# Kernel optimization log

Hardware: AMD Instinct MI355X
Metric: run time of the kernel (lower is better)

The kernel has to match this reference:

```python
import jax, jax.numpy as jnp
import numpy as np

B, S, F, OWN, H, E = 16384, 37, 17, 9, 256, 128
NOUT = 7 + 16


def setup_inputs() -> dict:
    key = jax.random.key(0)
    ks = jax.random.split(key, 22)
    obs = jax.random.normal(ks[0], (B, S + 1, F), dtype=jnp.float32)
    pad = jax.random.bernoulli(ks[1], 0.3, (B, S))
    obs = obs.at[:, 1:, :].multiply(jnp.where(pad, 0.0, 1.0)[:, :, None])

    def init(k, shape):
        return jax.random.normal(k, shape, dtype=jnp.float32) * 0.05

    params = dict(
        sW1=init(ks[2], (F, H)), sb1=jnp.zeros((H,), jnp.float32),
        sW2=init(ks[3], (H, H)), sb2=jnp.zeros((H,), jnp.float32),
        sW3=init(ks[4], (H, E)), sb3=jnp.zeros((E,), jnp.float32),
        aW1=init(ks[5], (E + OWN, H)), ab1=jnp.zeros((H,), jnp.float32),
        aW2=init(ks[6], (H, H)), ab2=jnp.zeros((H,), jnp.float32),
        aW3=init(ks[7], (H, NOUT)), ab3=jnp.zeros((NOUT,), jnp.float32),
        vW1=init(ks[8], (E + OWN, H)), vb1=jnp.zeros((H,), jnp.float32),
        vW2=init(ks[9], (H, H)), vb2=jnp.zeros((H,), jnp.float32),
        vW3=init(ks[10], (H, 1)), vb3=jnp.zeros((1,), jnp.float32),
    )
    return {"obs": obs, **params}


def reference(obs, sW1, sb1, sW2, sb2, sW3, sb3,
              aW1, ab1, aW2, ab2, aW3, ab3,
              vW1, vb1, vW2, vb2, vW3, vb3):
    s_own = obs[:, 0, :OWN]                      # [B, 9]
    seqs = obs[:, 1:, :]                         # [B, 37, 17]
    # non-padded mask: rows whose abs-sum is nonzero
    mask = (jnp.sum(jnp.abs(seqs), axis=-1) != 0).astype(obs.dtype)  # [B, 37]

    # shared MLP applied to every row; masked positions zeroed before the
    # pooling sum (equivalent to gather->MLP->scatter into zeros->sum)
    h = jax.nn.relu(seqs @ sW1 + sb1)
    h = jax.nn.relu(h @ sW2 + sb2)
    h = jax.nn.relu(h @ sW3 + sb3)               # [B, 37, E]
    h = h * mask[..., None]
    summed = jnp.sum(h, axis=1)                  # [B, E]

    cat = jnp.concatenate([summed, s_own], axis=1)  # [B, E+9]

    a = jax.nn.relu(cat @ aW1 + ab1)
    a = jax.nn.relu(a @ aW2 + ab2)
    action_logits = a @ aW3 + ab3                # [B, 23]

    v = jax.nn.relu(cat @ vW1 + vb1)
    v = jax.nn.relu(v @ vW2 + vb2)
    value = (v @ vW3 + vb3).reshape(-1)          # [B]

    return action_logits, value
```

## Files before the change

kernel.cpp:

```cpp
#include <hip/hip_runtime.h>
#include <hip/hip_bf16.h>

#define B_    16384
#define S_    37
#define F_    17
#define OWN_  9
#define NOUT_ 23
#define OBS_ROW 646

typedef __bf16 bf16x8 __attribute__((ext_vector_type(8)));
typedef float  f32x4  __attribute__((ext_vector_type(4)));

#define MFMA(a,b,c) __builtin_amdgcn_mfma_f32_16x16x32_bf16(a, b, c, 0, 0, 0)

#define W1F_OFF   0
#define W2F_OFF   8192
#define W3F_OFF   73728
#define AW1F_OFF  106496
#define AW2F_OFF  147456
#define AW3F_OFF  212992
#define VW1F_OFF  221184
#define VW2F_OFF  262144
#define VW3F_OFF  327680
#define PREP_TOTAL 331776

__global__ void prep_kernel(const float* __restrict__ sW1, const float* __restrict__ sW2,
                            const float* __restrict__ sW3, const float* __restrict__ aW1,
                            const float* __restrict__ aW2, const float* __restrict__ aW3,
                            const float* __restrict__ vW1, const float* __restrict__ vW2,
                            const float* __restrict__ vW3, __bf16* __restrict__ ws)
{
    int j = blockIdx.x * 256 + threadIdx.x;
    const float* src; __bf16* dst; int Np, Ks, Ns;
    if (j < 8192)                  { dst = ws + W1F_OFF;  src = sW1; Np = 256; Ks = 17;  Ns = 256; }
    else if ((j -= 8192)  < 65536) { dst = ws + W2F_OFF;  src = sW2; Np = 256; Ks = 256; Ns = 256; }
    else if ((j -= 65536) < 32768) { dst = ws + W3F_OFF;  src = sW3; Np = 128; Ks = 256; Ns = 128; }
    else if ((j -= 32768) < 40960) { dst = ws + AW1F_OFF; src = aW1; Np = 256; Ks = 137; Ns = 256; }
    else if ((j -= 40960) < 65536) { dst = ws + AW2F_OFF; src = aW2; Np = 256; Ks = 256; Ns = 256; }
    else if ((j -= 65536) < 8192)  { dst = ws + AW3F_OFF; src = aW3; Np = 32;  Ks = 256; Ns = 23;  }
    else if ((j -= 8192)  < 40960) { dst = ws + VW1F_OFF; src = vW1; Np = 256; Ks = 137; Ns = 256; }
    else if ((j -= 40960) < 65536) { dst = ws + VW2F_OFF; src = vW2; Np = 256; Ks = 256; Ns = 256; }
    else { j -= 65536;               dst = ws + VW3F_OFF; src = vW3; Np = 16;  Ks = 256; Ns = 1;   }
    const int c = j / (Np * 8), rem = j - c * Np * 8, n = rem >> 3, e = rem & 7, k = c * 8 + e;
    const float v = (k < Ks && n < Ns) ? src[k * Ns + n] : 0.f;
    dst[j] = (__bf16)v;
}

__global__ __launch_bounds__(512, 2) void fused_kernel(
    const float* __restrict__ obs,
    const float* __restrict__ sb1, const float* __restrict__ sb2, const float* __restrict__ sb3,
    const float* __restrict__ ab1, const float* __restrict__ ab2, const float* __restrict__ ab3,
    const float* __restrict__ vb1, const float* __restrict__ vb2, const float* __restrict__ vb3,
    const __bf16* __restrict__ ws, float* __restrict__ out)
{
    __shared__ __align__(16) char pool[74240];
    __bf16* act1 = (__bf16*)pool;
    __bf16* act2 = (__bf16*)(pool + 32768);
    __bf16* xs0  = (__bf16*)(pool + 65536);
    __bf16* xs1  = (__bf16*)(pool + 69632);
    float*  sm0  = (float*)(pool + 73728);
    float*  sm1  = (float*)(pool + 73984);
    __bf16* catf = (__bf16*)(pool + 65536);

    const __bf16* W1f  = ws + W1F_OFF;
    const __bf16* W2f  = ws + W2F_OFF;
    const __bf16* W3f  = ws + W3F_OFF;
    const __bf16* AW1f = ws + AW1F_OFF;
    const __bf16* AW2f = ws + AW2F_OFF;
    const __bf16* AW3f = ws + AW3F_OFF;
    const __bf16* VW1f = ws + VW1F_OFF;
    const __bf16* VW2f = ws + VW2F_OFF;
    const __bf16* VW3f = ws + VW3F_OFF;

    const int tid  = threadIdx.x;
    const int wave = tid >> 6;
    const int lane = tid & 63;
    const int q    = lane >> 4;
    const int l16  = lane & 15;
    const int b0   = blockIdx.x * 16;
    const f32x4 z4 = {0.f, 0.f, 0.f, 0.f};

    for (int i = tid; i < 4096; i += 512) xs0[i] = (__bf16)0.f;

    bf16x8 w1f[2], w2f[8][2], w3f[8];
    float b1v[2], b2v[2];
    #pragma unroll
    for (int nt = 0; nt < 2; ++nt) {
        const int n = wave * 32 + nt * 16 + l16;
        w1f[nt] = *(const bf16x8*)(W1f + ((size_t)q * 256 + n) * 8);
        b1v[nt] = sb1[n];
        b2v[nt] = sb2[n];
        #pragma unroll
        for (int k = 0; k < 8; ++k)
            w2f[k][nt] = *(const bf16x8*)(W2f + ((size_t)(k * 4 + q) * 256 + n) * 8);
    }
    #pragma unroll
    for (int k = 0; k < 8; ++k)
        w3f[k] = *(const bf16x8*)(W3f + ((size_t)(k * 4 + q) * 128 + wave * 16 + l16) * 8);
    const float b3v = sb3[wave * 16 + l16];

    __syncthreads();

    if (wave == 7) {
        const float* p = obs + (size_t)(b0 + (lane & 15)) * OBS_ROW + ((lane >> 4) + 1) * F_;
        float sm = 0.f;
        #pragma unroll
        for (int c = 0; c < F_; ++c) {
            const float v = p[c];
            sm += fabsf(v);
            xs0[((c >> 3) * 64 + lane) * 8 + (c & 7)] = (__bf16)v;
        }
        sm0[lane] = sm;
    }

    f32x4 vsum = z4;

    for (int it = 0; it < 10; ++it) {
        __bf16* xc  = (it & 1) ? xs1 : xs0;
        __bf16* xn  = (it & 1) ? xs0 : xs1;
        float*  smc = (it & 1) ? sm1 : sm0;
        float*  smn = (it & 1) ? sm0 : sm1;

        __syncthreads();

        if (it < 9 && wave == 7) {
            const int s = 4 * (it + 1) + (lane >> 4);
            if (s < S_) {
                const float* p = obs + (size_t)(b0 + (lane & 15)) * OBS_ROW + (s + 1) * F_;
                float sm = 0.f;
                #pragma unroll
                for (int c = 0; c < F_; ++c) {
                    const float v = p[c];
                    sm += fabsf(v);
                    xn[((c >> 3) * 64 + lane) * 8 + (c & 7)] = (__bf16)v;
                }
                smn[lane] = sm;
            } else {
                smn[lane] = 0.f;
            }
        }

        {
            #pragma unroll
            for (int m = 0; m < 4; ++m) {
                const bf16x8 af = *(const bf16x8*)(xc + (q * 64 + m * 16 + l16) * 8);
                #pragma unroll
                for (int nt = 0; nt < 2; ++nt) {
                    const f32x4 h = MFMA(af, w1f[nt], z4);
                    const int n = wave * 32 + nt * 16 + l16, c = n >> 3, e = n & 7;
                    #pragma unroll
                    for (int r = 0; r < 4; ++r) {
                        float v = h[r] + b1v[nt]; v = v > 0.f ? v : 0.f;
                        act1[(c * 64 + m * 16 + q * 4 + r) * 8 + e] = (__bf16)v;
                    }
                }
            }
        }
        __syncthreads();

        {
            f32x4 h2[2][4];
            #pragma unroll
            for (int nt = 0; nt < 2; ++nt)
                #pragma unroll
                for (int m = 0; m < 4; ++m) h2[nt][m] = z4;
            #pragma unroll
            for (int k = 0; k < 8; ++k) {
                const int k8 = k * 4 + q;
                #pragma unroll
                for (int m = 0; m < 4; ++m) {
                    const bf16x8 a = *(const bf16x8*)(act1 + (k8 * 64 + m * 16 + l16) * 8);
                    h2[0][m] = MFMA(a, w2f[k][0], h2[0][m]);
                    h2[1][m] = MFMA(a, w2f[k][1], h2[1][m]);
                }
            }
            #pragma unroll
            for (int nt = 0; nt < 2; ++nt) {
                const int n = wave * 32 + nt * 16 + l16, c = n >> 3, e = n & 7;
                #pragma unroll
                for (int m = 0; m < 4; ++m)
                    #pragma unroll
                    for (int r = 0; r < 4; ++r) {
                        float v = h2[nt][m][r] + b2v[nt]; v = v > 0.f ? v : 0.f;
                        act2[(c * 64 + m * 16 + q * 4 + r) * 8 + e] = (__bf16)v;
                    }
            }
        }
        __syncthreads();

        {
            f32x4 h3[4];
            #pragma unroll
            for (int m = 0; m < 4; ++m) h3[m] = z4;
            #pragma unroll
            for (int k = 0; k < 8; ++k) {
                const int k8 = k * 4 + q;
                #pragma unroll
                for (int m = 0; m < 4; ++m) {
                    const bf16x8 a = *(const bf16x8*)(act2 + (k8 * 64 + m * 16 + l16) * 8);
                    h3[m] = MFMA(a, w3f[k], h3[m]);
                }
            }
            #pragma unroll
            for (int m = 0; m < 4; ++m)
                #pragma unroll
                for (int r = 0; r < 4; ++r) {
                    const float mv = smc[m * 16 + q * 4 + r];
                    float v = h3[m][r] + b3v;
                    v = v > 0.f ? v : 0.f;
                    vsum[r] += (mv != 0.f) ? v : 0.f;
                }
    }
    }

    __syncthreads();

    if (tid < 16) {
        const float* p = obs + (size_t)(b0 + tid) * OBS_ROW;
        #pragma unroll
        for (int c = 0; c < 8; ++c) catf[(16 * 16 + tid) * 8 + c] = (__bf16)p[c];
        catf[(17 * 16 + tid) * 8 + 0] = (__bf16)p[8];
        #pragma unroll
        for (int c = 1; c < 8; ++c) catf[(17 * 16 + tid) * 8 + c] = (__bf16)0.f;
    } else if (tid < 32) {
        const int rr = tid - 16;
        #pragma unroll
        for (int c = 0; c < 8; ++c) {
            catf[(18 * 16 + rr) * 8 + c] = (__bf16)0.f;
            catf[(19 * 16 + rr) * 8 + c] = (__bf16)0.f;
        }
    }
    {
        const int col = wave * 16 + l16, c = col >> 3, e = col & 7;
        #pragma unroll
        for (int r = 0; r < 4; ++r)
            catf[(c * 16 + q * 4 + r) * 8 + e] = (__bf16)vsum[r];
    }
    __syncthreads();

    {
        f32x4 ha[2], hv[2];
        #pragma unroll
        for (int nt = 0; nt < 2; ++nt) { ha[nt] = z4; hv[nt] = z4; }
        #pragma unroll
        for (int k = 0; k < 5; ++k) {
            const int k8 = k * 4 + q;
            const bf16x8 ca = *(const bf16x8*)(catf + (k8 * 16 + l16) * 8);
            #pragma unroll
            for (int nt = 0; nt < 2; ++nt) {
                const int n = wave * 32 + nt * 16 + l16;
                const bf16x8 ba = *(const bf16x8*)(AW1f + ((size_t)k8 * 256 + n) * 8);
                const bf16x8 bv = *(const bf16x8*)(VW1f + ((size_t)k8 * 256 + n) * 8);
                ha[nt] = MFMA(ca, ba, ha[nt]);
                hv[nt] = MFMA(ca, bv, hv[nt]);
            }
        }
        #pragma unroll
        for (int nt = 0; nt < 2; ++nt) {
            const int n = wave * 32 + nt * 16 + l16, c = n >> 3, e = n & 7;
            const float ba_ = ab1[n], bv_ = vb1[n];
            #pragma unroll
            for (int r = 0; r < 4; ++r) {
                float va = ha[nt][r] + ba_; va = va > 0.f ? va : 0.f;
                float vv = hv[nt][r] + bv_; vv = vv > 0.f ? vv : 0.f;
                act1[(c * 64 + q * 4 + r) * 8 + e]      = (__bf16)va;
                act1[(c * 64 + 16 + q * 4 + r) * 8 + e] = (__bf16)vv;
            }
        }
    }
    __syncthreads();

    {
        f32x4 ha[2], hv[2];
        #pragma unroll
        for (int nt = 0; nt < 2; ++nt) { ha[nt] = z4; hv[nt] = z4; }
        #pragma unroll
        for (int k = 0; k < 8; ++k) {
            const int k8 = k * 4 + q;
            const bf16x8 a0 = *(const bf16x8*)(act1 + (k8 * 64 + l16) * 8);
            const bf16x8 a1 = *(const bf16x8*)(act1 + (k8 * 64 + 16 + l16) * 8);
            #pragma unroll
            for (int nt = 0; nt < 2; ++nt) {
                const int n = wave * 32 + nt * 16 + l16;
                const bf16x8 ba = *(const bf16x8*)(AW2f + ((size_t)k8 * 256 + n) * 8);
                const bf16x8 bv = *(const bf16x8*)(VW2f + ((size_t)k8 * 256 + n) * 8);
                ha[nt] = MFMA(a0, ba, ha[nt]);
                hv[nt] = MFMA(a1, bv, hv[nt]);
            }
        }
        #pragma unroll
        for (int nt = 0; nt < 2; ++nt) {
            const int n = wave * 32 + nt * 16 + l16, c = n >> 3, e = n & 7;
            const float ba_ = ab2[n], bv_ = vb2[n];
            #pragma unroll
            for (int r = 0; r < 4; ++r) {
                float va = ha[nt][r] + ba_; va = va > 0.f ? va : 0.f;
                float vv = hv[nt][r] + bv_; vv = vv > 0.f ? vv : 0.f;
                act2[(c * 64 + q * 4 + r) * 8 + e]      = (__bf16)va;
                act2[(c * 64 + 16 + q * 4 + r) * 8 + e] = (__bf16)vv;
            }
        }
    }
    __syncthreads();

    if (wave < 2) {
        f32x4 acc = z4;
        #pragma unroll
        for (int k = 0; k < 8; ++k) {
            const int k8 = k * 4 + q;
            const bf16x8 a0 = *(const bf16x8*)(act2 + (k8 * 64 + l16) * 8);
            const bf16x8 bf = *(const bf16x8*)(AW3f + ((size_t)k8 * 32 + wave * 16 + l16) * 8);
            acc = MFMA(a0, bf, acc);
        }
        const int col = wave * 16 + l16;
        if (col < NOUT_) {
            const float bb = ab3[col];
            #pragma unroll
            for (int r = 0; r < 4; ++r)
                out[(size_t)(b0 + q * 4 + r) * NOUT_ + col] = acc[r] + bb;
        }
    } else if (wave == 2) {
        f32x4 acc = z4;
        #pragma unroll
        for (int k = 0; k < 8; ++k) {
            const int k8 = k * 4 + q;
            const bf16x8 a1 = *(const bf16x8*)(act2 + (k8 * 64 + 16 + l16) * 8);
            const bf16x8 bf = *(const bf16x8*)(VW3f + ((size_t)k8 * 16 + l16) * 8);
            acc = MFMA(a1, bf, acc);
        }
        if (l16 == 0) {
            const float bb = vb3[0];
            #pragma unroll
            for (int r = 0; r < 4; ++r)
                out[(size_t)B_ * NOUT_ + b0 + q * 4 + r] = acc[r] + bb;
        }
    }
}

extern "C" void kernel_launch(void* const* d_in, const int* in_sizes, int n_in,
                              void* d_out, int out_size, void* d_ws, size_t ws_size,
                              hipStream_t stream)
{
    const float* obs = (const float*)d_in[0];
    const float* sW1 = (const float*)d_in[1];
    const float* sb1 = (const float*)d_in[2];
    const float* sW2 = (const float*)d_in[3];
    const float* sb2 = (const float*)d_in[4];
    const float* sW3 = (const float*)d_in[5];
    const float* sb3 = (const float*)d_in[6];
    const float* aW1 = (const float*)d_in[7];
    const float* ab1 = (const float*)d_in[8];
    const float* aW2 = (const float*)d_in[9];
    const float* ab2 = (const float*)d_in[10];
    const float* aW3 = (const float*)d_in[11];
    const float* ab3 = (const float*)d_in[12];
    const float* vW1 = (const float*)d_in[13];
    const float* vb1 = (const float*)d_in[14];
    const float* vW2 = (const float*)d_in[15];
    const float* vb2 = (const float*)d_in[16];
    const float* vW3 = (const float*)d_in[17];
    const float* vb3 = (const float*)d_in[18];

    __bf16* ws = (__bf16*)d_ws;
    float* out = (float*)d_out;

    hipLaunchKernelGGL(prep_kernel, dim3(PREP_TOTAL / 256), dim3(256), 0, stream,
                       sW1, sW2, sW3, aW1, aW2, aW3, vW1, vW2, vW3, ws);
    hipLaunchKernelGGL(fused_kernel, dim3(B_ / 16), dim3(512), 0, stream,
                       obs, sb1, sb2, sb3, ab1, ab2, ab3, vb1, vb2, vb3,
                       (const __bf16*)ws, out);
}
```

Baseline: 281.9 us.

## Switch MFMA operand order to row-major padded LDS layout and regroup wave tiling

Changes the shared-memory activation layout from chunked k8-major to row-major with padded row strides, so the bank-conflict pattern changes. MFMA operands are swapped so each lane writes four contiguous bf16 outputs as one vector store. The tiling is regrouped so each wave covers 64 output columns and 32 rows rather than 32 columns and 64 rows. Biases are staged in shared memory, and the actor and value heads are split across the two wave halves. The aim is cheaper LDS stores and fewer bank conflicts, at the cost of roughly twice the register-resident weight fragments per wave, which may hurt occupancy.

```diff
diff --git a/kernel.cpp b/kernel.cpp
--- a/kernel.cpp
+++ b/kernel.cpp
@@ -9,6 +9,7 @@
 #define OBS_ROW 646
 
 typedef __bf16 bf16x8 __attribute__((ext_vector_type(8)));
+typedef __bf16 bf16x4 __attribute__((ext_vector_type(4)));
 typedef float  f32x4  __attribute__((ext_vector_type(4)));
 
 #define MFMA(a,b,c) __builtin_amdgcn_mfma_f32_16x16x32_bf16(a, b, c, 0, 0, 0)
@@ -23,6 +24,10 @@
 #define VW2F_OFF  262144
 #define VW3F_OFF  327680
 #define PREP_TOTAL 331776
+
+#define RS_ACT 264
+#define RS_XS  40
+#define RS_CAT 168
 
 __global__ void prep_kernel(const float* __restrict__ sW1, const float* __restrict__ sW2,
                             const float* __restrict__ sW3, const float* __restrict__ aW1,
@@ -53,43 +58,37 @@
     const float* __restrict__ vb1, const float* __restrict__ vb2, const float* __restrict__ vb3,
     const __bf16* __restrict__ ws, float* __restrict__ out)
 {
-    __shared__ __align__(16) char pool[74240];
-    __bf16* act1 = (__bf16*)pool;
-    __bf16* act2 = (__bf16*)(pool + 32768);
-    __bf16* xs0  = (__bf16*)(pool + 65536);
-    __bf16* xs1  = (__bf16*)(pool + 69632);
-    float*  sm0  = (float*)(pool + 73728);
-    float*  sm1  = (float*)(pool + 73984);
-    __bf16* catf = (__bf16*)(pool + 65536);
+    __shared__ __align__(16) __bf16 act1[64 * RS_ACT];
+    __shared__ __align__(16) __bf16 act2[64 * RS_ACT];
+    __shared__ __align__(16) __bf16 xs[2][64 * RS_XS];
+    __shared__ float sm[2][64];
+    __shared__ __align__(16) float sbias[640];
+    __shared__ __align__(16) __bf16 catf[16 * RS_CAT];
 
     const __bf16* W1f  = ws + W1F_OFF;
     const __bf16* W2f  = ws + W2F_OFF;
     const __bf16* W3f  = ws + W3F_OFF;
-    const __bf16* AW1f = ws + AW1F_OFF;
-    const __bf16* AW2f = ws + AW2F_OFF;
-    const __bf16* AW3f = ws + AW3F_OFF;
-    const __bf16* VW1f = ws + VW1F_OFF;
-    const __bf16* VW2f = ws + VW2F_OFF;
-    const __bf16* VW3f = ws + VW3F_OFF;
 
     const int tid  = threadIdx.x;
     const int wave = tid >> 6;
     const int lane = tid & 63;
     const int q    = lane >> 4;
     const int l16  = lane & 15;
+    const int wg   = wave & 3;
+    const int th   = wave >> 2;
+    const int tb   = th * 32;
     const int b0   = blockIdx.x * 16;
     const f32x4 z4 = {0.f, 0.f, 0.f, 0.f};
 
-    for (int i = tid; i < 4096; i += 512) xs0[i] = (__bf16)0.f;
-
-    bf16x8 w1f[2], w2f[8][2], w3f[8];
-    float b1v[2], b2v[2];
+    for (int i = tid; i < 640; i += 512)
+        sbias[i] = (i < 256) ? sb1[i] : (i < 512 ? sb2[i - 256] : sb3[i - 512]);
+    for (int i = tid; i < 2 * 64 * RS_XS; i += 512) xs[0][i] = (__bf16)0.f;
+
+    bf16x8 w1f[4], w2f[8][4], w3f[8];
     #pragma unroll
-    for (int nt = 0; nt < 2; ++nt) {
-        const int n = wave * 32 + nt * 16 + l16;
+    for (int nt = 0; nt < 4; ++nt) {
+        const int n = wg * 64 + nt * 16 + l16;
         w1f[nt] = *(const bf16x8*)(W1f + ((size_t)q * 256 + n) * 8);
-        b1v[nt] = sb1[n];
-        b2v[nt] = sb2[n];
         #pragma unroll
         for (int k = 0; k < 8; ++k)
             w2f[k][nt] = *(const bf16x8*)(W2f + ((size_t)(k * 4 + q) * 256 + n) * 8);
@@ -97,93 +96,99 @@
     #pragma unroll
     for (int k = 0; k < 8; ++k)
         w3f[k] = *(const bf16x8*)(W3f + ((size_t)(k * 4 + q) * 128 + wave * 16 + l16) * 8);
-    const float b3v = sb3[wave * 16 + l16];
 
     __syncthreads();
 
     if (wave == 7) {
         const float* p = obs + (size_t)(b0 + (lane & 15)) * OBS_ROW + ((lane >> 4) + 1) * F_;
-        float sm = 0.f;
+        float smv = 0.f;
         #pragma unroll
         for (int c = 0; c < F_; ++c) {
             const float v = p[c];
-            sm += fabsf(v);
-            xs0[((c >> 3) * 64 + lane) * 8 + (c & 7)] = (__bf16)v;
-        }
-        sm0[lane] = sm;
-    }
+            smv += fabsf(v);
+            xs[0][lane * RS_XS + c] = (__bf16)v;
+        }
+        sm[0][lane] = smv;
+    }
+    __syncthreads();
 
     f32x4 vsum = z4;
 
     for (int it = 0; it < 10; ++it) {
-        __bf16* xc  = (it & 1) ? xs1 : xs0;
-        __bf16* xn  = (it & 1) ? xs0 : xs1;
-        float*  smc = (it & 1) ? sm1 : sm0;
-        float*  smn = (it & 1) ? sm0 : sm1;
-
-        __syncthreads();
+        const __bf16* xc = xs[it & 1];
+        __bf16*       xn = xs[1 - (it & 1)];
+        const float* smc = sm[it & 1];
+        float*       smn = sm[1 - (it & 1)];
 
         if (it < 9 && wave == 7) {
             const int s = 4 * (it + 1) + (lane >> 4);
             if (s < S_) {
                 const float* p = obs + (size_t)(b0 + (lane & 15)) * OBS_ROW + (s + 1) * F_;
-                float sm = 0.f;
+                float smv = 0.f;
                 #pragma unroll
                 for (int c = 0; c < F_; ++c) {
                     const float v = p[c];
-                    sm += fabsf(v);
-                    xn[((c >> 3) * 64 + lane) * 8 + (c & 7)] = (__bf16)v;
-                }
-                smn[lane] = sm;
+                    smv += fabsf(v);
+                    xn[lane * RS_XS + c] = (__bf16)v;
+                }
+                smn[lane] = smv;
             } else {
                 smn[lane] = 0.f;
             }
         }
 
         {
-            #pragma unroll
-            for (int m = 0; m < 4; ++m) {
-                const bf16x8 af = *(const bf16x8*)(xc + (q * 64 + m * 16 + l16) * 8);
-                #pragma unroll
-                for (int nt = 0; nt < 2; ++nt) {
-                    const f32x4 h = MFMA(af, w1f[nt], z4);
-                    const int n = wave * 32 + nt * 16 + l16, c = n >> 3, e = n & 7;
+            bf16x8 xa[2];
+            #pragma unroll
+            for (int tt = 0; tt < 2; ++tt)
+                xa[tt] = *(const bf16x8*)(xc + (tb + tt * 16 + l16) * RS_XS + q * 8);
+            #pragma unroll
+            for (int nt = 0; nt < 4; ++nt) {
+                const int n0 = wg * 64 + nt * 16 + q * 4;
+                const f32x4 bb = *(const f32x4*)(sbias + n0);
+                #pragma unroll
+                for (int tt = 0; tt < 2; ++tt) {
+                    const f32x4 h = MFMA(w1f[nt], xa[tt], z4);
+                    bf16x4 o;
                     #pragma unroll
                     for (int r = 0; r < 4; ++r) {
-                        float v = h[r] + b1v[nt]; v = v > 0.f ? v : 0.f;
-                        act1[(c * 64 + m * 16 + q * 4 + r) * 8 + e] = (__bf16)v;
+                        float v = h[r] + bb[r];
+                        o[r] = (__bf16)(v > 0.f ? v : 0.f);
                     }
+                    *(bf16x4*)(act1 + (tb + tt * 16 + l16) * RS_ACT + n0) = o;
                 }
             }
         }
         __syncthreads();
 
         {
-            f32x4 h2[2][4];
-            #pragma unroll
-            for (int nt = 0; nt < 2; ++nt)
-                #pragma unroll
-                for (int m = 0; m < 4; ++m) h2[nt][m] = z4;
+            f32x4 acc[4][2];
+            #pragma unroll
+            for (int nt = 0; nt < 4; ++nt) { acc[nt][0] = z4; acc[nt][1] = z4; }
             #pragma unroll
             for (int k = 0; k < 8; ++k) {
-                const int k8 = k * 4 + q;
-                #pragma unroll
-                for (int m = 0; m < 4; ++m) {
-                    const bf16x8 a = *(const bf16x8*)(act1 + (k8 * 64 + m * 16 + l16) * 8);
-                    h2[0][m] = MFMA(a, w2f[k][0], h2[0][m]);
-                    h2[1][m] = MFMA(a, w2f[k][1], h2[1][m]);
-                }
-            }
-            #pragma unroll
-            for (int nt = 0; nt < 2; ++nt) {
-                const int n = wave * 32 + nt * 16 + l16, c = n >> 3, e = n & 7;
-                #pragma unroll
-                for (int m = 0; m < 4; ++m)
+                const bf16x8 a0 = *(const bf16x8*)(act1 + (tb + l16) * RS_ACT + k * 32 + q * 8);
+                const bf16x8 a1 = *(const bf16x8*)(act1 + (tb + 16 + l16) * RS_ACT + k * 32 + q * 8);
+                #pragma unroll
+                for (int nt = 0; nt < 4; ++nt) {
+                    acc[nt][0] = MFMA(w2f[k][nt], a0, acc[nt][0]);
+                    acc[nt][1] = MFMA(w2f[k][nt], a1, acc[nt][1]);
+                }
+            }
+            #pragma unroll
+            for (int nt = 0; nt < 4; ++nt) {
+                const int n0 = wg * 64 + nt * 16 + q * 4;
+                const f32x4 bb = *(const f32x4*)(sbias + 256 + n0);
+                #pragma unroll
+                for (int tt = 0; tt < 2; ++tt) {
+                    bf16x4 o;
                     #pragma unroll
                     for (int r = 0; r < 4; ++r) {
-                        float v = h2[nt][m][r] + b2v[nt]; v = v > 0.f ? v : 0.f;
-                        act2[(c * 64 + m * 16 + q * 4 + r) * 8 + e] = (__bf16)v;
+                        float v = acc[nt][tt][r] + bb[r];
+                        o[r] = (__bf16)(v > 0.f ? v : 0.f);
                     }
+                    *(bf16x4*)(act2 + (tb + tt * 16 + l16) * RS_ACT + n0) = o;
+                }
             }
         }
         __syncthreads();
@@ -194,111 +199,100 @@
             for (int m = 0; m < 4; ++m) h3[m] = z4;
             #pragma unroll
             for (int k = 0; k < 8; ++k) {
-                const int k8 = k * 4 + q;
                 #pragma unroll
                 for (int m = 0; m < 4; ++m) {
-                    const bf16x8 a = *(const bf16x8*)(act2 + (k8 * 64 + m * 16 + l16) * 8);
-                    h3[m] = MFMA(a, w3f[k], h3[m]);
-                }
-            }
-            #pragma unroll
-            for (int m = 0; m < 4; ++m)
+                    const bf16x8 a = *(const bf16x8*)(act2 + (m * 16 + l16) * RS_ACT + k * 32 + q * 8);
+                    h3[m] = MFMA(w3f[k], a, h3[m]);
+                }
+            }
+            const f32x4 bb = *(const f32x4*)(sbias + 512 + wave * 16 + q * 4);
+            #pragma unroll
+            for (int m = 0; m < 4; ++m) {
+                const float mv = smc[m * 16 + l16];
                 #pragma unroll
                 for (int r = 0; r < 4; ++r) {
-                    const float mv = smc[m * 16 + q * 4 + r];
-                    float v = h3[m][r] + b3v;
+                    float v = h3[m][r] + bb[r];
                     v = v > 0.f ? v : 0.f;
                     vsum[r] += (mv != 0.f) ? v : 0.f;
                 }
-    }
-    }
-
-    __syncthreads();
-
+            }
+        }
+    }
+
+    {
+        bf16x4 o;
+        #pragma unroll
+        for (int r = 0; r < 4; ++r) o[r] = (__bf16)vsum[r];
+        *(bf16x4*)(catf + l16 * RS_CAT + wave * 16 + q * 4) = o;
+    }
     if (tid < 16) {
         const float* p = obs + (size_t)(b0 + tid) * OBS_ROW;
         #pragma unroll
-        for (int c = 0; c < 8; ++c) catf[(16 * 16 + tid) * 8 + c] = (__bf16)p[c];
-        catf[(17 * 16 + tid) * 8 + 0] = (__bf16)p[8];
-        #pragma unroll
-        for (int c = 1; c < 8; ++c) catf[(17 * 16 + tid) * 8 + c] = (__bf16)0.f;
-    } else if (tid < 32) {
-        const int rr = tid - 16;
-        #pragma unroll
-        for (int c = 0; c < 8; ++c) {
-            catf[(18 * 16 + rr) * 8 + c] = (__bf16)0.f;
-            catf[(19 * 16 + rr) * 8 + c] = (__bf16)0.f;
-        }
-    }
+        for (int j = 0; j < OWN_; ++j) catf[tid * RS_CAT + 128 + j] = (__bf16)p[j];
+        #pragma unroll
+        for (int j = OWN_; j < 32; ++j) catf[tid * RS_CAT + 128 + j] = (__bf16)0.f;
+    }
+    __syncthreads();
+
+    const bool  actor = (wave < 4);
+    const int   drow  = actor ? l16 : (16 + l16);
+    const __bf16* HW1 = ws + (actor ? AW1F_OFF : VW1F_OFF);
+    const __bf16* HW2 = ws + (actor ? AW2F_OFF : VW2F_OFF);
+    const float* hb1  = actor ? ab1 : vb1;
+    const float* hb2  = actor ? ab2 : vb2;
+
     {
-        const int col = wave * 16 + l16, c = col >> 3, e = col & 7;
-        #pragma unroll
-        for (int r = 0; r < 4; ++r)
-            catf[(c * 16 + q * 4 + r) * 8 + e] = (__bf16)vsum[r];
+        f32x4 acc[4];
+        #pragma unroll
+        for (int nt = 0; nt < 4; ++nt) acc[nt] = z4;
+        #pragma unroll
+        for (int k = 0; k < 5; ++k) {
+            const bf16x8 ca = *(const bf16x8*)(catf + l16 * RS_CAT + k * 32 + q * 8);
+            #pragma unroll
+            for (int nt = 0; nt < 4; ++nt) {
+                const bf16x8 wf = *(const bf16x8*)(HW1 + ((size_t)(k * 4 + q) * 256 + wg * 64 + nt * 16 + l16) * 8);
+                acc[nt] = MFMA(wf, ca, acc[nt]);
+            }
+        }
+        #pragma unroll
+        for (int nt = 0; nt < 4; ++nt) {
+            const int n0 = wg * 64 + nt * 16 + q * 4;
+            const f32x4 bb = *(const f32x4*)(hb1 + n0);
+            bf16x4 o;
+            #pragma unroll
+            for (int r = 0; r < 4; ++r) {
+                float v = acc[nt][r] + bb[r];
+                o[r] = (__bf16)(v > 0.f ? v : 0.f);
+            }
+            *(bf16x4*)(act1 + drow * RS_ACT + n0) = o;
+        }
     }
     __syncthreads();
 
     {
-        f32x4 ha[2], hv[2];
-        #pragma unroll
-        for (int nt = 0; nt < 2; ++nt) { ha[nt] = z4; hv[nt] = z4; }
-        #pragma unroll
-        for (int k = 0; k < 5; ++k) {
-            const int k8 = k * 4 + q;
-            const bf16x8 ca = *(const bf16x8*)(catf + (k8 * 16 + l16) * 8);
-            #pragma unroll
-            for (int nt = 0; nt < 2; ++nt) {
-                const int n = wave * 32 + nt * 16 + l16;
-                const bf16x8 ba = *(const bf16x8*)(AW1f + ((size_t)k8 * 256 + n) * 8);
-                const bf16x8 bv = *(const bf16x8*)(VW1f + ((size_t)k8 * 256 + n) * 8);
-                ha[nt] = MFMA(ca, ba, ha[nt]);
-                hv[nt] = MFMA(ca, bv, hv[nt]);
-            }
-        }
-        #pragma unroll
-        for (int nt = 0; nt < 2; ++nt) {
-            const int n = wave * 32 + nt * 16 + l16, c = n >> 3, e = n & 7;
-            const float ba_ = ab1[n], bv_ = vb1[n];
+        f32x4 acc[4];
+        #pragma unroll
+        for (int nt = 0; nt < 4; ++nt) acc[nt] = z4;
+        #pragma unroll
+        for (int k = 0; k < 8; ++k) {
+            const bf16x8 a = *(const bf16x8*)(act1 + drow * RS_ACT + k * 32 + q * 8);
+            #pragma unroll
+            for (int nt = 0; nt < 4; ++nt) {
+                const bf16x8 wf = *(const bf16x8*)(HW2 + ((size_t)(k * 4 + q) * 256 + wg * 64 + nt * 16 + l16) * 8);
+                acc[nt] = MFMA(wf, a, acc[nt]);
+            }
+        }
+        #pragma unroll
+        for (int nt = 0; nt < 4; ++nt) {
+            const int n0 = wg * 64 + nt * 16 + q * 4;
+            const f32x4 bb = *(const f32x4*)(hb2 + n0);
+            bf16x4 o;
             #pragma unroll
             for (int r = 0; r < 4; ++r) {
-                float va = ha[nt][r] + ba_; va = va > 0.f ? va : 0.f;
-                float vv = hv[nt][r] + bv_; vv = vv > 0.f ? vv : 0.f;
-                act1[(c * 64 + q * 4 + r) * 8 + e]      = (__bf16)va;
-                act1[(c * 64 + 16 + q * 4 + r) * 8 + e] = (__bf16)vv;
-            }
-        }
-    }
-    __syncthreads();
-
-    {
-        f32x4 ha[2], hv[2];
-        #pragma unroll
-        for (int nt = 0; nt < 2; ++nt) { ha[nt] = z4; hv[nt] = z4; }
-        #pragma unroll
-        for (int k = 0; k < 8; ++k) {
-            const int k8 = k * 4 + q;
-            const bf16x8 a0 = *(const bf16x8*)(act1 + (k8 * 64 + l16) * 8);
-            const bf16x8 a1 = *(const bf16x8*)(act1 + (k8 * 64 + 16 + l16) * 8);
-            #pragma unroll
-            for (int nt = 0; nt < 2; ++nt) {
-                const int n = wave * 32 + nt * 16 + l16;
-                const bf16x8 ba = *(const bf16x8*)(AW2f + ((size_t)k8 * 256 + n) * 8);
-                const bf16x8 bv = *(const bf16x8*)(VW2f + ((size_t)k8 * 256 + n) * 8);
-                ha[nt] = MFMA(a0, ba, ha[nt]);
-                hv[nt] = MFMA(a1, bv, hv[nt]);
-            }
-        }
-        #pragma unroll
-        for (int nt = 0; nt < 2; ++nt) {
-            const int n = wave * 32 + nt * 16 + l16, c = n >> 3, e = n & 7;
-            const float ba_ = ab2[n], bv_ = vb2[n];
-            #pragma unroll
-            for (int r = 0; r < 4; ++r) {
-                float va = ha[nt][r] + ba_; va = va > 0.f ? va : 0.f;
-                float vv = hv[nt][r] + bv_; vv = vv > 0.f ? vv : 0.f;
-                act2[(c * 64 + q * 4 + r) * 8 + e]      = (__bf16)va;
-                act2[(c * 64 + 16 + q * 4 + r) * 8 + e] = (__bf16)vv;
-            }
+                float v = acc[nt][r] + bb[r];
+                o[r] = (__bf16)(v > 0.f ? v : 0.f);
+            }
+            *(bf16x4*)(act2 + drow * RS_ACT + n0) = o;
         }
     }
     __syncthreads();
@@ -307,33 +301,26 @@
         f32x4 acc = z4;
         #pragma unroll
         for (int k = 0; k < 8; ++k) {
-            const int k8 = k * 4 + q;
-            const bf16x8 a0 = *(const bf16x8*)(act2 + (k8 * 64 + l16) * 8);
-            const bf16x8 bf = *(const bf16x8*)(AW3f + ((size_t)k8 * 32 + wave * 16 + l16) * 8);
-            acc = MFMA(a0, bf, acc);
-        }
-        const int col = wave * 16 + l16;
-        if (col < NOUT_) {
-            const float bb = ab3[col];
-            #pragma unroll
-            for (int r = 0; r < 4; ++r)
-                out[(size_t)(b0 + q * 4 + r) * NOUT_ + col] = acc[r] + bb;
-        }
-    } else if (wave == 2) {
+            const bf16x8 a  = *(const bf16x8*)(act2 + l16 * RS_ACT + k * 32 + q * 8);
+            const bf16x8 wf = *(const bf16x8*)(ws + AW3F_OFF + ((size_t)(k * 4 + q) * 32 + wave * 16 + l16) * 8);
+            acc = MFMA(wf, a, acc);
+        }
+        #pragma unroll
+        for (int r = 0; r < 4; ++r) {
+            const int logit = wave * 16 + q * 4 + r;
+            if (logit < NOUT_)
+                out[(size_t)(b0 + l16) * NOUT_ + logit] = acc[r] + ab3[logit];
+        }
+    } else if (wave == 4) {
         f32x4 acc = z4;
         #pragma unroll
         for (int k = 0; k < 8; ++k) {
-            const int k8 = k * 4 + q;
-            const bf16x8 a1 = *(const bf16x8*)(act2 + (k8 * 64 + 16 + l16) * 8);
-            const bf16x8 bf = *(const bf16x8*)(VW3f + ((size_t)k8 * 16 + l16) * 8);
-            acc = MFMA(a1, bf, acc);
-        }
-        if (l16 == 0) {
-            const float bb = vb3[0];
-            #pragma unroll
-            for (int r = 0; r < 4; ++r)
-                out[(size_t)B_ * NOUT_ + b0 + q * 4 + r] = acc[r] + bb;
-        }
+            const bf16x8 a  = *(const bf16x8*)(act2 + (16 + l16) * RS_ACT + k * 32 + q * 8);
+            const bf16x8 wf = *(const bf16x8*)(ws + VW3F_OFF + ((size_t)(k * 4 + q) * 16 + l16) * 8);
+            acc = MFMA(wf, a, acc);
+        }
+        if (q == 0)
+            out[(size_t)B_ * NOUT_ + b0 + l16] = acc[0] + vb3[0];
     }
 }
 
```

Result: slower. 296.7 us (+5.3%).
